# Kernel tuning notes

Measured on AMD Instinct MI355X. Metric: run time of the kernel, lower is better.

Reference implementation:

```python
import jax, jax.numpy as jnp
import numpy as np

BN_EPS = 1e-5
POOL_TARGETS = (1500, 750, 375)


def mesh_conv(x, nb, W, g, b):
    # x: (E, C), nb: (E, 4), W: (5*C, Cout)
    E, C = x.shape
    n = x[jnp.clip(nb, 0, E - 1)]              # (E, 4, C) gather
    p1 = jnp.sort(n[:, :2, :], axis=1)          # symmetrize face-pair 1
    p2 = jnp.sort(n[:, 2:, :], axis=1)          # symmetrize face-pair 2
    feat = jnp.concatenate([x, p1[:, 0], p1[:, 1], p2[:, 0], p2[:, 1]], axis=1)  # (E, 5C)
    h = feat @ W                                # (E, Cout)
    mu = h.mean(axis=0)
    var = h.var(axis=0)                         # biased var (BatchNorm training stats)
    h = (h - mu) * jax.lax.rsqrt(var + BN_EPS) * g + b
    return jax.nn.relu(h)


def mesh_pool(x, nb, target):
    E = x.shape[0]
    scores = jnp.linalg.norm(x, axis=1)
    keep = jnp.sort(jnp.argsort(-scores)[:target])          # (target,) sorted kept edges
    x_pool = x[keep]
    remap = jnp.full((E,), -1, dtype=jnp.int32).at[keep].set(jnp.arange(target, dtype=jnp.int32))
    nbr = remap[jnp.clip(nb[keep], 0, E - 1)]               # (target, 4)
    self_idx = jnp.broadcast_to(jnp.arange(target, dtype=jnp.int32)[:, None], nbr.shape)
    nb_pool = jnp.where(nbr < 0, self_idx, nbr)
    return x_pool, nb_pool, keep


def mesh_unpool(x_coarse, keep, E_fine):
    # keep is sorted ascending; nearest kept edge by integer index distance
    # (ties -> lower index, matching torch argmin-first semantics).
    idx = jnp.arange(E_fine)
    pos = jnp.searchsorted(keep, idx)
    K = keep.shape[0]
    left = jnp.clip(pos - 1, 0, K - 1)
    right = jnp.clip(pos, 0, K - 1)
    dl = jnp.abs(idx - keep[left])
    dr = jnp.abs(idx - keep[right])
    nn_idx = jnp.where(dl <= dr, left, right)
    return x_coarse[nn_idx]                                 # kept edges map to themselves (d=0)


def setup_inputs() -> dict:
    key = jax.random.key(0)
    ks = jax.random.split(key, 20)
    E = 200000
    x = jax.random.normal(ks[0], (E, 5), dtype=jnp.float32)
    nb = jax.random.randint(ks[1], (E, 4), 0, E, dtype=jnp.int64)

    def lin(k, cin, cout):
        return (jax.random.normal(k, (cin, cout), dtype=jnp.float32) * 0.05)

    dims = [(5, 64), (64, 128), (128, 256), (256, 512), (768, 256), (384, 128), (192, 64)]
    names = ['e1', 'e2', 'e3', 'e4', 'd3', 'd2', 'd1']
    inp = {'x': x, 'nb': nb}
    for i, ((cin, cout), nm) in enumerate(zip(dims, names)):
        inp['W_' + nm] = lin(ks[2 + i], cin * 5, cout)
        inp['g_' + nm] = jnp.ones((cout,), dtype=jnp.float32)
        inp['b_' + nm] = jnp.zeros((cout,), dtype=jnp.float32)
    inp['W_head'] = lin(ks[12], 64, 4)
    inp['bias_head'] = jnp.zeros((4,), dtype=jnp.float32)
    return inp


def _forward(x, nb,
             W_e1, g_e1, b_e1, W_e2, g_e2, b_e2, W_e3, g_e3, b_e3, W_e4, g_e4, b_e4,
             W_d3, g_d3, b_d3, W_d2, g_d2, b_d2, W_d1, g_d1, b_d1,
             W_head, bias_head):
    e1 = mesh_conv(x, nb, W_e1, g_e1, b_e1)
    e1p, nb1, keep1 = mesh_pool(e1, nb, POOL_TARGETS[0])
    e2 = mesh_conv(e1p, nb1, W_e2, g_e2, b_e2)
    e2p, nb2, keep2 = mesh_pool(e2, nb1, POOL_TARGETS[1])
    e3 = mesh_conv(e2p, nb2, W_e3, g_e3, b_e3)
    e3p, nb3, keep3 = mesh_pool(e3, nb2, POOL_TARGETS[2])
    e4 = mesh_conv(e3p, nb3, W_e4, g_e4, b_e4)
    d3 = mesh_unpool(e4, keep3, e3.shape[0])
    d3 = mesh_conv(jnp.concatenate([d3, e3], axis=1), nb2, W_d3, g_d3, b_d3)
    d2 = mesh_unpool(d3, keep2, e2.shape[0])
    d2 = mesh_conv(jnp.concatenate([d2, e2], axis=1), nb1, W_d2, g_d2, b_d2)
    d1 = mesh_unpool(d2, keep1, e1.shape[0])
    d1 = mesh_conv(jnp.concatenate([d1, e1], axis=1), nb, W_d1, g_d1, b_d1)
    return d1 @ W_head + bias_head


def reference(x, nb,
              W_e1, g_e1, b_e1, W_e2, g_e2, b_e2, W_e3, g_e3, b_e3, W_e4, g_e4, b_e4,
              W_d3, g_d3, b_d3, W_d2, g_d2, b_d2, W_d1, g_d1, b_d1,
              W_head, bias_head):
    return _forward(x, nb,
                    W_e1, g_e1, b_e1, W_e2, g_e2, b_e2, W_e3, g_e3, b_e3, W_e4, g_e4, b_e4,
                    W_d3, g_d3, b_d3, W_d2, g_d2, b_d2, W_d1, g_d1, b_d1,
                    W_head, bias_head)
```

## Files before the change

### kernel.cpp

```cpp
#include <hip/hip_runtime.h>
#include <stdint.h>

typedef unsigned long long u64;
typedef unsigned int u32;
typedef unsigned short ushort_t;

#define FI __device__ __forceinline__

static constexpr float BN_EPS_F = 1e-5f;
static constexpr int E0 = 200000;
static constexpr int T1 = 1500, T2 = 750, T3 = 375;
static constexpr int CAND_CAP = 4096;
static constexpr int NB_KEEP = (E0 + 1023) / 1024;

typedef __attribute__((ext_vector_type(8))) short short8;
typedef __attribute__((ext_vector_type(4))) float f32x4;

FI int iclampi(int v, int lo, int hi) { return v < lo ? lo : (v > hi ? hi : v); }

FI ushort_t f2b(float f) {
  u32 u = __float_as_uint(f);
  u32 r = (u + 0x7FFFu + ((u >> 16) & 1u)) >> 16;
  return (ushort_t)r;
}

FI void u16minmax(const uint4& va, const uint4& vb, uint4& lo, uint4& hi) {
  const ushort_t* a = (const ushort_t*)&va;
  const ushort_t* b = (const ushort_t*)&vb;
  ushort_t* l = (ushort_t*)&lo;
  ushort_t* h = (ushort_t*)&hi;
  #pragma unroll
  for (int i = 0; i < 8; i++) {
    ushort_t x = a[i], y = b[i];
    l[i] = x < y ? x : y;
    h[i] = x < y ? y : x;
  }
}

FI int nearest_keep(const int* __restrict__ keep, int K, int idx) {
  int lo = 0, hi = K;
  while (lo < hi) { int mid = (lo + hi) >> 1; if (keep[mid] < idx) lo = mid + 1; else hi = mid; }
  int l = lo - 1; l = l < 0 ? 0 : (l > K - 1 ? K - 1 : l);
  int r = lo;     r = r < 0 ? 0 : (r > K - 1 ? K - 1 : r);
  int dl = idx - keep[l]; dl = dl < 0 ? -dl : dl;
  int dr = idx - keep[r]; dr = dr < 0 ? -dr : dr;
  return (dl <= dr) ? l : r;
}

FI int bsearch_eq(const int* __restrict__ keep, int K, int v) {
  int lo = 0, hi = K;
  while (lo < hi) { int mid = (lo + hi) >> 1; if (keep[mid] < v) lo = mid + 1; else hi = mid; }
  if (lo < K && keep[lo] == v) return lo;
  return -1;
}

template<int C, int Cout, int BR, int BC, int KT, int TR, int TC, int KSPLIT,
         bool FUSE_STATS>
__global__ __launch_bounds__((BR / TR) * (BC / TC))
void conv_kernel(const float* __restrict__ X,
                 const int* __restrict__ nb, int E,
                 const float* __restrict__ W,
                 float* __restrict__ H, float* __restrict__ stats)
{
  constexpr int NTH = (BR / TR) * (BC / TC);
  constexpr int VK = 5 * KT;
  constexpr int KC = C / KSPLIT;
  static_assert(KC % KT == 0, "KC % KT");

  const int row0 = blockIdx.x * BR;
  const int col0 = blockIdx.y * BC;
  const int c_begin = (KSPLIT > 1) ? (int)blockIdx.z * KC : 0;

  __shared__ float As[VK][BR];
  __shared__ float Bs[VK][BC];
  __shared__ int rowsS[5][BR];
  __shared__ float red[FUSE_STATS ? 2 * (BR / TR) * BC : 1];

  const int tid = threadIdx.x;

  for (int q = tid; q < BR; q += NTH) {
    int r = row0 + q;
    int rr[5];
    if (r < E) {
      rr[0] = r;
      #pragma unroll
      for (int j = 0; j < 4; j++) {
        int v = nb[(size_t)r * 4 + j];
        rr[1 + j] = iclampi(v, 0, E - 1);
      }
    } else {
      #pragma unroll
      for (int j = 0; j < 5; j++) rr[j] = -1;
    }
    #pragma unroll
    for (int j = 0; j < 5; j++) rowsS[j][q] = rr[j];
  }

  float acc[TR][TC];
  #pragma unroll
  for (int i = 0; i < TR; i++)
    #pragma unroll
    for (int j = 0; j < TC; j++) acc[i][j] = 0.f;

  const int tr = tid / (BC / TC);
  const int tc = tid % (BC / TC);
  const int rA = tr * TR;
  const int cB = tc * TC;

  for (int c0 = c_begin; c0 < c_begin + KC; c0 += KT) {
    __syncthreads();
    for (int q = tid; q < VK * (BC / 4); q += NTH) {
      int kk = q / (BC / 4);
      int c4 = q % (BC / 4);
      int p = kk / KT, t = kk % KT;
      float4 wv = *(const float4*)&W[(size_t)(p * C + c0 + t) * Cout + col0 + c4 * 4];
      *(float4*)&Bs[kk][c4 * 4] = wv;
    }
    for (int q = tid; q < BR * KT; q += NTH) {
      int t = q % KT, rq = q / KT;
      int c = c0 + t;
      float s0 = 0.f, a1 = 0.f, a2 = 0.f, a3 = 0.f, a4 = 0.f;
      if (rowsS[0][rq] >= 0) {
        float v0, v1, v2, v3;
        s0 = X[(size_t)rowsS[0][rq] * C + c];
        v0 = X[(size_t)rowsS[1][rq] * C + c];
        v1 = X[(size_t)rowsS[2][rq] * C + c];
        v2 = X[(size_t)rowsS[3][rq] * C + c];
        v3 = X[(size_t)rowsS[4][rq] * C + c];
        a1 = fminf(v0, v1); a2 = fmaxf(v0, v1);
        a3 = fminf(v2, v3); a4 = fmaxf(v2, v3);
      }
      As[0 * KT + t][rq] = s0;
      As[1 * KT + t][rq] = a1;
      As[2 * KT + t][rq] = a2;
      As[3 * KT + t][rq] = a3;
      As[4 * KT + t][rq] = a4;
    }
    __syncthreads();

    for (int kk = 0; kk < VK; kk++) {
      float a[TR], b[TC];
      #pragma unroll
      for (int i = 0; i < TR; i++) a[i] = As[kk][rA + i];
      #pragma unroll
      for (int j = 0; j < TC; j++) b[j] = Bs[kk][cB + j];
      #pragma unroll
      for (int i = 0; i < TR; i++)
        #pragma unroll
        for (int j = 0; j < TC; j++)
          acc[i][j] = fmaf(a[i], b[j], acc[i][j]);
    }
  }

  #pragma unroll
  for (int i = 0; i < TR; i++) {
    int r = row0 + rA + i;
    if (r < E) {
      if constexpr (KSPLIT > 1) {
        #pragma unroll
        for (int j = 0; j < TC; j++)
          atomicAdd(&H[(size_t)r * Cout + col0 + cB + j], acc[i][j]);
      } else {
        #pragma unroll
        for (int j = 0; j < TC; j += 4) {
          float4 v = make_float4(acc[i][j], acc[i][j + 1], acc[i][j + 2], acc[i][j + 3]);
          *(float4*)&H[(size_t)r * Cout + col0 + cB + j] = v;
        }
      }
    }
  }

  if constexpr (FUSE_STATS) {
    float s[TC], q2[TC];
    #pragma unroll
    for (int j = 0; j < TC; j++) { s[j] = 0.f; q2[j] = 0.f; }
    #pragma unroll
    for (int i = 0; i < TR; i++) {
      int r = row0 + rA + i;
      if (r < E) {
        #pragma unroll
        for (int j = 0; j < TC; j++) { float v = acc[i][j]; s[j] += v; q2[j] += v * v; }
      }
    }
    __syncthreads();
    float* redS = &red[0];
    float* redQ = &red[(BR / TR) * BC];
    #pragma unroll
    for (int j = 0; j < TC; j++) {
      redS[tr * BC + cB + j] = s[j];
      redQ[tr * BC + cB + j] = q2[j];
    }
    __syncthreads();
    for (int col = tid; col < BC; col += NTH) {
      float ts = 0.f, tq = 0.f;
      for (int g = 0; g < BR / TR; g++) { ts += redS[g * BC + col]; tq += redQ[g * BC + col]; }
      atomicAdd(&stats[col0 + col], ts);
      atomicAdd(&stats[Cout + col0 + col], tq);
    }
  }
}

__global__ __launch_bounds__(256)
void e1_conv_kernel(const float* __restrict__ X, const int* __restrict__ nb,
                    const float* __restrict__ W,
                    float* __restrict__ H, float* __restrict__ stats)
{
  __shared__ float As[25][128];
  __shared__ float Bs[25][64];
  __shared__ float red[2 * 32 * 64];

  const int tid = threadIdx.x;
  const int row0 = (int)blockIdx.x * 128;

  if (tid < 128) {
    int r = row0 + tid; if (r > E0 - 1) r = E0 - 1;
    int rs[5];
    rs[0] = r;
    #pragma unroll
    for (int j = 0; j < 4; j++) rs[1 + j] = iclampi((int)nb[(size_t)r * 4 + j], 0, E0 - 1);
    float v[5][5];
    #pragma unroll
    for (int j = 0; j < 5; j++) {
      const float* src = &X[(size_t)rs[j] * 5];
      float4 a = *(const float4*)src;
      v[j][0] = a.x; v[j][1] = a.y; v[j][2] = a.z; v[j][3] = a.w;
      v[j][4] = src[4];
    }
    #pragma unroll
    for (int c = 0; c < 5; c++) {
      As[0 * 5 + c][tid] = v[0][c];
      As[1 * 5 + c][tid] = fminf(v[1][c], v[2][c]);
      As[2 * 5 + c][tid] = fmaxf(v[1][c], v[2][c]);
      As[3 * 5 + c][tid] = fminf(v[3][c], v[4][c]);
      As[4 * 5 + c][tid] = fmaxf(v[3][c], v[4][c]);
    }
  } else {
    for (int q = tid - 128; q < 25 * 16; q += 128) {
      int k = q / 16, c4 = q % 16;
      float4 wv = *(const float4*)&W[(size_t)k * 64 + c4 * 4];
      *(float4*)&Bs[k][c4 * 4] = wv;
    }
  }
  __syncthreads();

  const int tr = tid >> 3;
  const int tc = tid & 7;
  const int rA = tr * 4;
  const int cB = tc * 8;

  float acc[4][8];
  #pragma unroll
  for (int i = 0; i < 4; i++)
    #pragma unroll
    for (int j = 0; j < 8; j++) acc[i][j] = 0.f;

  for (int k = 0; k < 25; k++) {
    float a[4], b[8];
    #pragma unroll
    for (int i = 0; i < 4; i++) a[i] = As[k][rA + i];
    #pragma unroll
    for (int j = 0; j < 8; j++) b[j] = Bs[k][cB + j];
    #pragma unroll
    for (int i = 0; i < 4; i++)
      #pragma unroll
      for (int j = 0; j < 8; j++)
        acc[i][j] = fmaf(a[i], b[j], acc[i][j]);
  }

  float s[8], q2[8];
  #pragma unroll
  for (int j = 0; j < 8; j++) { s[j] = 0.f; q2[j] = 0.f; }
  #pragma unroll
  for (int i = 0; i < 4; i++) {
    int r = row0 + rA + i;
    if (r < E0) {
      #pragma unroll
      for (int j = 0; j < 8; j += 4) {
        float4 v = make_float4(acc[i][j], acc[i][j + 1], acc[i][j + 2], acc[i][j + 3]);
        *(float4*)&H[(size_t)r * 64 + cB + j] = v;
      }
      #pragma unroll
      for (int j = 0; j < 8; j++) { float v = acc[i][j]; s[j] += v; q2[j] += v * v; }
    }
  }
  __syncthreads();
  float* redS = &red[0];
  float* redQ = &red[32 * 64];
  #pragma unroll
  for (int j = 0; j < 8; j++) {
    redS[tr * 64 + cB + j] = s[j];
    redQ[tr * 64 + cB + j] = q2[j];
  }
  __syncthreads();
  for (int col = tid; col < 64; col += 256) {
    float ts = 0.f, tq = 0.f;
    for (int g = 0; g < 32; g++) { ts += redS[g * 64 + col]; tq += redQ[g * 64 + col]; }
    atomicAdd(&stats[col], ts);
    atomicAdd(&stats[64 + col], tq);
  }
}

template<int C, int Cout>
__global__ __launch_bounds__(128)
void mfma_conv_kernel(const ushort_t* __restrict__ src,
                      const int* __restrict__ nb, int E,
                      const ushort_t* __restrict__ Wt,
                      float* __restrict__ H, float* __restrict__ stats)
{
  constexpr int NCC = C / 32;
  __shared__ int rows[5][32];

  const int tid = threadIdx.x;
  const int lane = tid & 63;
  const int wv = tid >> 6;
  const int l15 = lane & 15;
  const int quad = lane >> 4;
  const int row0 = (int)blockIdx.x * 32;
  const int col0 = (int)blockIdx.y * 64;

  if (tid < 32) {
    int r = row0 + tid; if (r > E - 1) r = E - 1;
    rows[0][tid] = r;
    #pragma unroll
    for (int j = 0; j < 4; j++) rows[1 + j][tid] = iclampi(nb[(size_t)r * 4 + j], 0, E - 1);
  }
  __syncthreads();

  const int rr = wv * 16 + l15;
  int r5[5];
  #pragma unroll
  for (int j = 0; j < 5; j++) r5[j] = rows[j][rr];

  f32x4 acc[4];
  #pragma unroll
  for (int ni = 0; ni < 4; ni++) acc[ni] = (f32x4){0.f, 0.f, 0.f, 0.f};

  uint4 raw[2][5];
  auto loadcc = [&](int par, int cc2) {
    int cb = cc2 * 32 + quad * 8;
    #pragma unroll
    for (int j = 0; j < 5; j++)
      raw[par][j] = *(const uint4*)&src[(size_t)r5[j] * C + cb];
  };

  loadcc(0, 0);
  #pragma unroll
  for (int cc = 0; cc < NCC; cc++) {
    const int par = cc & 1;
    if (cc + 1 < NCC) loadcc(par ^ 1, cc + 1);
    short8 a[5];
    a[0] = *(short8*)&raw[par][0];
    {
      uint4 lo, hi;
      u16minmax(raw[par][1], raw[par][2], lo, hi);
      a[1] = *(short8*)&lo; a[2] = *(short8*)&hi;
    }
    {
      uint4 lo, hi;
      u16minmax(raw[par][3], raw[par][4], lo, hi);
      a[3] = *(short8*)&lo; a[4] = *(short8*)&hi;
    }
    #pragma unroll
    for (int p = 0; p < 5; p++) {
      #pragma unroll
      for (int ni = 0; ni < 4; ni++) {
        short8 bf = *(const short8*)&Wt[((size_t)(p * Cout + col0 + ni * 16 + l15)) * C + cc * 32 + quad * 8];
        acc[ni] = __builtin_amdgcn_mfma_f32_16x16x32_bf16(a[p], bf, acc[ni], 0, 0, 0);
      }
    }
  }

  float s[4] = {0.f, 0.f, 0.f, 0.f}, q[4] = {0.f, 0.f, 0.f, 0.f};
  #pragma unroll
  for (int reg = 0; reg < 4; reg++) {
    int r = row0 + wv * 16 + quad * 4 + reg;
    if (r < E) {
      #pragma unroll
      for (int ni = 0; ni < 4; ni++) {
        float v = acc[ni][reg];
        H[(size_t)r * Cout + col0 + ni * 16 + l15] = v;
        s[ni] += v; q[ni] += v * v;
      }
    }
  }
  #pragma unroll
  for (int ni = 0; ni < 4; ni++) {
    float ts = s[ni], tq = q[ni];
    ts += __shfl_xor(ts, 16); tq += __shfl_xor(tq, 16);
    ts += __shfl_xor(ts, 32); tq += __shfl_xor(tq, 32);
    if (quad == 0) {
      int col = col0 + ni * 16 + l15;
      atomicAdd(&stats[col], ts);
      atomicAdd(&stats[Cout + col], tq);
    }
  }
}

__global__ __launch_bounds__(256, 4)
void d1_mfma_kernel(const ushort_t* __restrict__ d2b, const ushort_t* __restrict__ e1b,
                    const int* __restrict__ nn1, const int* __restrict__ nb,
                    const ushort_t* __restrict__ Wt,
                    float* __restrict__ H, float* __restrict__ stats)
{
  __shared__ int rowsD[5][128];
  __shared__ int rowsS[5][128];

  const int tid = threadIdx.x;
  const int lane = tid & 63;
  const int wv = tid >> 6;
  const int l15 = lane & 15;
  const int quad = lane >> 4;
  const int row0 = (int)blockIdx.x * 128;

  if (tid < 128) {
    int r = row0 + tid; if (r > E0 - 1) r = E0 - 1;
    int rs[5];
    rs[0] = r;
    #pragma unroll
    for (int j = 0; j < 4; j++) rs[1 + j] = iclampi((int)nb[(size_t)r * 4 + j], 0, E0 - 1);
    #pragma unroll
    for (int j = 0; j < 5; j++) { rowsS[j][tid] = rs[j]; rowsD[j][tid] = nn1[rs[j]]; }
  }
  __syncthreads();

  f32x4 acc[8];
  #pragma unroll
  for (int mi = 0; mi < 8; mi++) acc[mi] = (f32x4){0.f, 0.f, 0.f, 0.f};

  for (int cc = 0; cc < 6; cc++) {
    const bool fromD = cc < 4;
    const ushort_t* __restrict__ src = fromD ? d2b : e1b;
    const int stride = fromD ? 128 : 64;
    const int cbase = (fromD ? cc * 32 : (cc - 4) * 32) + quad * 8;

    short8 bf[5];
    #pragma unroll
    for (int p = 0; p < 5; p++)
      bf[p] = *(const short8*)&Wt[((size_t)(p * 64 + wv * 16 + l15)) * 192 + cc * 32 + quad * 8];

    #pragma unroll 2
    for (int mi = 0; mi < 8; mi++) {
      int rr = mi * 16 + l15;
      int r0, r1, r2, r3, r4;
      if (fromD) {
        r0 = rowsD[0][rr]; r1 = rowsD[1][rr]; r2 = rowsD[2][rr];
        r3 = rowsD[3][rr]; r4 = rowsD[4][rr];
      } else {
        r0 = rowsS[0][rr]; r1 = rowsS[1][rr]; r2 = rowsS[2][rr];
        r3 = rowsS[3][rr]; r4 = rowsS[4][rr];
      }
      uint4 v0 = *(const uint4*)&src[(size_t)r0 * stride + cbase];
      uint4 v1 = *(const uint4*)&src[(size_t)r1 * stride + cbase];
      uint4 v2 = *(const uint4*)&src[(size_t)r2 * stride + cbase];
      uint4 v3 = *(const uint4*)&src[(size_t)r3 * stride + cbase];
      uint4 v4 = *(const uint4*)&src[(size_t)r4 * stride + cbase];

      uint4 lo12, hi12, lo34, hi34;
      u16minmax(v1, v2, lo12, hi12);
      u16minmax(v3, v4, lo34, hi34);

      acc[mi] = __builtin_amdgcn_mfma_f32_16x16x32_bf16(*(short8*)&v0,   bf[0], acc[mi], 0, 0, 0);
      acc[mi] = __builtin_amdgcn_mfma_f32_16x16x32_bf16(*(short8*)&lo12, bf[1], acc[mi], 0, 0, 0);
      acc[mi] = __builtin_amdgcn_mfma_f32_16x16x32_bf16(*(short8*)&hi12, bf[2], acc[mi], 0, 0, 0);
      acc[mi] = __builtin_amdgcn_mfma_f32_16x16x32_bf16(*(short8*)&lo34, bf[3], acc[mi], 0, 0, 0);
      acc[mi] = __builtin_amdgcn_mfma_f32_16x16x32_bf16(*(short8*)&hi34, bf[4], acc[mi], 0, 0, 0);
    }
  }

  const int col = wv * 16 + l15;
  float s = 0.f, q = 0.f;
  #pragma unroll
  for (int mi = 0; mi < 8; mi++) {
    #pragma unroll
    for (int reg = 0; reg < 4; reg++) {
      int r = row0 + mi * 16 + quad * 4 + reg;
      if (r < E0) {
        float v = acc[mi][reg];
        H[(size_t)r * 64 + col] = v;
        s += v; q += v * v;
      }
    }
  }
  s += __shfl_xor(s, 16); q += __shfl_xor(q, 16);
  s += __shfl_xor(s, 32); q += __shfl_xor(q, 32);
  if (quad == 0) {
    atomicAdd(&stats[col], s);
    atomicAdd(&stats[64 + col], q);
  }
}

template<int C, int Cout>
__global__ void prep_w_kernel(const float* __restrict__ W, ushort_t* __restrict__ Wt)
{
  int idx = (int)blockIdx.x * 256 + threadIdx.x;
  if (idx < 5 * C * Cout) {
    int n = idx % Cout;
    int k = idx / Cout;
    int p = k / C, c = k % C;
    Wt[((size_t)(p * Cout + n)) * C + c] = f2b(W[(size_t)k * Cout + n]);
  }
}

__global__ void stats_kernel(const float* __restrict__ H, int E, int Cout,
                             float* __restrict__ stats)
{
  const int RB = 64;
  int r0 = (int)blockIdx.x * RB;
  int rend = r0 + RB; if (rend > E) rend = E;
  for (int col = threadIdx.x; col < Cout; col += blockDim.x) {
    float s = 0.f, q = 0.f;
    for (int r = r0; r < rend; r++) { float v = H[(size_t)r * Cout + col]; s += v; q += v * v; }
    atomicAdd(&stats[col], s);
    atomicAdd(&stats[Cout + col], q);
  }
}

template<int Cout, bool KEYS, bool B16>
__global__ void bn_kernel(const float* __restrict__ H, const float* __restrict__ stats,
                          const float* __restrict__ g, const float* __restrict__ b,
                          int E, float* __restrict__ Out, ushort_t* __restrict__ Outb,
                          u64* __restrict__ keys)
{
  constexpr int CPL = Cout / 64;
  const int lane = threadIdx.x & 63;
  const int wid = threadIdx.x >> 6;
  const int wpb = blockDim.x >> 6;
  const float invE = 1.0f / (float)E;
  float mu[CPL], inv[CPL], gg[CPL], bb[CPL];
  #pragma unroll
  for (int u = 0; u < CPL; u++) {
    int c = lane + u * 64;
    float m = stats[c] * invE;
    float var = stats[Cout + c] * invE - m * m;
    mu[u] = m;
    inv[u] = rsqrtf(var + BN_EPS_F);
    gg[u] = g[c]; bb[u] = b[c];
  }
  for (int r = (int)blockIdx.x * wpb + wid; r < E; r += (int)gridDim.x * wpb) {
    float ss = 0.f;
    #pragma unroll
    for (int u = 0; u < CPL; u++) {
      int c = lane + u * 64;
      float v = H[(size_t)r * Cout + c];
      float o = (v - mu[u]) * inv[u] * gg[u] + bb[u];
      o = fmaxf(o, 0.f);
      Out[(size_t)r * Cout + c] = o;
      if constexpr (B16) Outb[(size_t)r * Cout + c] = f2b(o);
      ss += o * o;
    }
    if constexpr (KEYS) {
      #pragma unroll
      for (int s = 32; s > 0; s >>= 1) ss += __shfl_xor(ss, s, 64);
      if (lane == 0) {
        float sc = sqrtf(ss);
        u32 sb = __float_as_uint(sc);
        keys[r] = ((u64)sb << 32) | (u64)(0xFFFFFFFFu - (u32)r);
      }
    }
  }
}

__global__ void head_kernel(const float* __restrict__ H, const float* __restrict__ stats,
                            const float* __restrict__ g, const float* __restrict__ b,
                            const float* __restrict__ Wh, const float* __restrict__ bh,
                            int E, float* __restrict__ out)
{
  const int lane = threadIdx.x & 63;
  const int wid = threadIdx.x >> 6;
  const int wpb = blockDim.x >> 6;
  const float invE = 1.0f / (float)E;
  float m = stats[lane] * invE;
  float var = stats[64 + lane] * invE - m * m;
  float inv = rsqrtf(var + BN_EPS_F);
  float gg = g[lane], bb = b[lane];
  float4 w = *(const float4*)&Wh[lane * 4];
  float b0 = bh[0], b1 = bh[1], b2 = bh[2], b3 = bh[3];
  for (int r = (int)blockIdx.x * wpb + wid; r < E; r += (int)gridDim.x * wpb) {
    float v = H[(size_t)r * 64 + lane];
    float o = fmaxf((v - m) * inv * gg + bb, 0.f);
    float a0 = o * w.x, a1 = o * w.y, a2 = o * w.z, a3 = o * w.w;
    #pragma unroll
    for (int s = 32; s > 0; s >>= 1) {
      a0 += __shfl_xor(a0, s, 64);
      a1 += __shfl_xor(a1, s, 64);
      a2 += __shfl_xor(a2, s, 64);
      a3 += __shfl_xor(a3, s, 64);
    }
    if (lane == 0) {
      float4 ov = make_float4(a0 + b0, a1 + b1, a2 + b2, a3 + b3);
      *(float4*)&out[(size_t)r * 4] = ov;
    }
  }
}

__global__ void hist_kernel(const u64* __restrict__ keys, int E, u32* __restrict__ hist)
{
  for (int i = (int)blockIdx.x * blockDim.x + threadIdx.x; i < E;
       i += (int)gridDim.x * blockDim.x) {
    u32 bin = (u32)(keys[i] >> 44);
    atomicAdd(&hist[bin], 1u);
  }
}

__global__ void scan_kernel(const u32* __restrict__ hist, int K, u32* __restrict__ sel)
{
  __shared__ u32 csum[1024];
  __shared__ u32 sb2[1024];
  __shared__ int selChunk;
  __shared__ u32 aboveChunk;
  const int tid = threadIdx.x;
  {
    const uint4* hp = (const uint4*)(hist + (size_t)tid * 1024);
    u32 s = 0;
    for (int i = 0; i < 256; i++) {
      uint4 v = hp[i];
      s += v.x + v.y + v.z + v.w;
    }
    csum[tid] = s;
  }
  __syncthreads();
  if (tid == 0) {
    u32 above = 0; int sc = 0; u32 ab = 0;
    for (int t = 1023; t >= 0; t--) {
      if (above + csum[t] >= (u32)K) { sc = t; ab = above; break; }
      above += csum[t];
    }
    selChunk = sc; aboveChunk = ab;
  }
  __syncthreads();
  sb2[tid] = hist[(size_t)selChunk * 1024 + tid];
  __syncthreads();
  if (tid == 0) {
    u32 above = aboveChunk; int sb = 0;
    for (int t = 1023; t >= 0; t--) {
      u32 c = sb2[t];
      if (above + c >= (u32)K) { sb = t; break; }
      above += c;
    }
    sel[0] = (u32)(selChunk * 1024 + sb);
    sel[1] = above;
    sel[2] = (u32)K - above;
  }
}

__global__ void collect_kernel(const u64* __restrict__ keys, int E, const u32* __restrict__ sel,
                               u64* __restrict__ cand, u32* __restrict__ count)
{
  u32 bin = sel[0];
  for (int i = (int)blockIdx.x * blockDim.x + threadIdx.x; i < E;
       i += (int)gridDim.x * blockDim.x) {
    if ((u32)(keys[i] >> 44) == bin) {
      u32 p = atomicAdd(count, 1u);
      if (p < (u32)CAND_CAP) cand[p] = keys[i];
    }
  }
}

__global__ void thresh_kernel(const u64* __restrict__ cand, const u32* __restrict__ count,
                              const u32* __restrict__ sel, u64* __restrict__ thr)
{
  __shared__ u64 sk[CAND_CAP];
  const int tid = threadIdx.x;
  const int nth = blockDim.x;
  int n = (int)(*count > (u32)CAND_CAP ? (u32)CAND_CAP : *count);
  int n2 = 2; while (n2 < n) n2 <<= 1;
  for (int i = tid; i < n2; i += nth) sk[i] = (i < n) ? cand[i] : 0ull;
  __syncthreads();
  for (int k = 2; k <= n2; k <<= 1)
    for (int j = k >> 1; j > 0; j >>= 1) {
      for (int i = tid; i < n2; i += nth) {
        int p = i ^ j;
        if (p > i) {
          u64 a = sk[i], bb = sk[p];
          bool up = ((i & k) == 0);
          bool sw = up ? (a < bb) : (a > bb);
          if (sw) { sk[i] = bb; sk[p] = a; }
        }
      }
      __syncthreads();
    }
  if (tid == 0) {
    int kr = (int)sel[2];
    thr[0] = sk[kr - 1];
  }
}

__global__ void keep_count_kernel(const u64* __restrict__ keys, int E,
                                  const u64* __restrict__ thrp, u32* __restrict__ bcnt)
{
  const u64 thr = thrp[0];
  const int tid = threadIdx.x;
  int base = (int)blockIdx.x * 1024 + tid * 4;
  u32 c = 0;
  #pragma unroll
  for (int u = 0; u < 4; u++) {
    int i = base + u;
    if (i < E && keys[i] >= thr) c++;
  }
  __shared__ u32 sm[256];
  sm[tid] = c;
  __syncthreads();
  for (int s = 128; s > 0; s >>= 1) {
    if (tid < s) sm[tid] += sm[tid + s];
    __syncthreads();
  }
  if (tid == 0) bcnt[blockIdx.x] = sm[0];
}

__global__ void keep_scan_kernel(const u32* __restrict__ bcnt, int NB, u32* __restrict__ boffs)
{
  __shared__ u32 sm[256];
  const int tid = threadIdx.x;
  u32 v = (tid < NB) ? bcnt[tid] : 0;
  sm[tid] = v;
  __syncthreads();
  for (int off = 1; off < 256; off <<= 1) {
    u32 t = 0;
    if (tid >= off) t = sm[tid - off];
    __syncthreads();
    sm[tid] += t;
    __syncthreads();
  }
  if (tid < NB) boffs[tid] = sm[tid] - v;
}

__global__ void keep_scatter_kernel(const u64* __restrict__ keys, int E,
                                    const u64* __restrict__ thrp, const u32* __restrict__ boffs,
                                    int* __restrict__ keep, int K)
{
  const u64 thr = thrp[0];
  const int tid = threadIdx.x;
  int base = (int)blockIdx.x * 1024 + tid * 4;
  u32 f[4]; u32 c = 0;
  #pragma unroll
  for (int u = 0; u < 4; u++) {
    int i = base + u;
    f[u] = (i < E && keys[i] >= thr) ? 1u : 0u;
    c += f[u];
  }
  __shared__ u32 sm[256];
  sm[tid] = c;
  __syncthreads();
  for (int off = 1; off < 256; off <<= 1) {
    u32 t = 0;
    if (tid >= off) t = sm[tid - off];
    __syncthreads();
    sm[tid] += t;
    __syncthreads();
  }
  u32 pos = boffs[blockIdx.x] + sm[tid] - c;
  #pragma unroll
  for (int u = 0; u < 4; u++) {
    if (f[u]) {
      if (pos < (u32)K) keep[pos] = base + u;
      pos++;
    }
  }
}

template<int NPOW>
__global__ void pool_select_kernel(const u64* __restrict__ keys, int E, int K,
                                   int* __restrict__ keep)
{
  __shared__ u64 sk[NPOW];
  __shared__ int si[NPOW];
  const int tid = threadIdx.x, nth = blockDim.x;
  for (int i = tid; i < NPOW; i += nth) sk[i] = (i < E) ? keys[i] : 0ull;
  __syncthreads();
  for (int k = 2; k <= NPOW; k <<= 1)
    for (int j = k >> 1; j > 0; j >>= 1) {
      for (int i = tid; i < NPOW; i += nth) {
        int p = i ^ j;
        if (p > i) {
          u64 a = sk[i], bb = sk[p];
          bool up = ((i & k) == 0);
          bool sw = up ? (a < bb) : (a > bb);
          if (sw) { sk[i] = bb; sk[p] = a; }
        }
      }
      __syncthreads();
    }
  for (int i = tid; i < NPOW; i += nth)
    si[i] = (i < K) ? (int)(0xFFFFFFFFu - (u32)(sk[i] & 0xFFFFFFFFull)) : 0x7FFFFFFF;
  __syncthreads();
  for (int k = 2; k <= NPOW; k <<= 1)
    for (int j = k >> 1; j > 0; j >>= 1) {
      for (int i = tid; i < NPOW; i += nth) {
        int p = i ^ j;
        if (p > i) {
          int a = si[i], bb = si[p];
          bool up = ((i & k) == 0);
          bool sw = up ? (a > bb) : (a < bb);
          if (sw) { si[i] = bb; si[p] = a; }
        }
      }
      __syncthreads();
    }
  for (int i = tid; i < K; i += nth) keep[i] = si[i];
}

template<int C, bool B16>
__global__ void pool_finish_kernel(const float* __restrict__ Xsrc, const int* __restrict__ nb_src,
                                   const int* __restrict__ keep, int K, int Esrc,
                                   float* __restrict__ Xp, ushort_t* __restrict__ Xpb,
                                   int* __restrict__ nbp)
{
  int total = K * C;
  for (int idx = (int)blockIdx.x * blockDim.x + threadIdx.x; idx < total;
       idx += (int)gridDim.x * blockDim.x) {
    int i = idx / C, c = idx % C;
    float v = Xsrc[(size_t)keep[i] * C + c];
    if constexpr (B16) Xpb[idx] = f2b(v);
    else Xp[idx] = v;
  }
  for (int idx = (int)blockIdx.x * blockDim.x + threadIdx.x; idx < K * 4;
       idx += (int)gridDim.x * blockDim.x) {
    int i = idx >> 2, j = idx & 3;
    int v = nb_src[(size_t)keep[i] * 4 + j];
    v = iclampi(v, 0, Esrc - 1);
    int p = bsearch_eq(keep, K, v);
    nbp[idx] = (p < 0) ? i : p;
  }
}

__global__ void unpool_cat_b16_kernel(const float* __restrict__ Xc, const float* __restrict__ Xs,
                                      const int* __restrict__ keep, int K, int E,
                                      int Cc, int Cs, ushort_t* __restrict__ out)
{
  int Ct = Cc + Cs;
  int total = E * Ct;
  for (int idx = (int)blockIdx.x * blockDim.x + threadIdx.x; idx < total;
       idx += (int)gridDim.x * blockDim.x) {
    int r = idx / Ct, c = idx % Ct;
    float v;
    if (c < Cc) { int nn = nearest_keep(keep, K, r); v = Xc[(size_t)nn * Cc + c]; }
    else v = Xs[(size_t)r * Cs + (c - Cc)];
    out[idx] = f2b(v);
  }
}

__global__ void nn_map_kernel(const int* __restrict__ keep, int K, int E, int* __restrict__ nn)
{
  for (int i = (int)blockIdx.x * blockDim.x + threadIdx.x; i < E;
       i += (int)gridDim.x * blockDim.x)
    nn[i] = nearest_keep(keep, K, i);
}

extern "C" void kernel_launch(void* const* d_in, const int* in_sizes, int n_in,
                              void* d_out, int out_size, void* d_ws, size_t ws_size,
                              hipStream_t stream)
{
  (void)in_sizes; (void)n_in; (void)out_size; (void)ws_size;
  const float* x     = (const float*)d_in[0];
  const int*   nb    = (const int*)d_in[1];
  const float* W_e1  = (const float*)d_in[2];
  const float* g_e1  = (const float*)d_in[3];
  const float* b_e1  = (const float*)d_in[4];
  const float* W_e2  = (const float*)d_in[5];
  const float* g_e2  = (const float*)d_in[6];
  const float* b_e2  = (const float*)d_in[7];
  const float* W_e3  = (const float*)d_in[8];
  const float* g_e3  = (const float*)d_in[9];
  const float* b_e3  = (const float*)d_in[10];
  const float* W_e4  = (const float*)d_in[11];
  const float* g_e4  = (const float*)d_in[12];
  const float* b_e4  = (const float*)d_in[13];
  const float* W_d3  = (const float*)d_in[14];
  const float* g_d3  = (const float*)d_in[15];
  const float* b_d3  = (const float*)d_in[16];
  const float* W_d2  = (const float*)d_in[17];
  const float* g_d2  = (const float*)d_in[18];
  const float* b_d2  = (const float*)d_in[19];
  const float* W_d1  = (const float*)d_in[20];
  const float* g_d1  = (const float*)d_in[21];
  const float* b_d1  = (const float*)d_in[22];
  const float* W_head = (const float*)d_in[23];
  const float* bias_head = (const float*)d_in[24];
  float* out = (float*)d_out;

  char* p = (char*)d_ws;
  auto alloc = [&](size_t bytes) -> char* {
    char* q = p; p += (bytes + 255) & ~(size_t)255; return q;
  };

  char* zz = p;
  u32*   hist  = (u32*)alloc(sizeof(u32) * (1u << 20));
  float* stats = (float*)alloc(sizeof(float) * 2 * (64 + 128 + 256 + 512 + 256 + 128 + 64));
  u32*   ctrl  = (u32*)alloc(sizeof(u32) * 16);
  u64*   thr   = (u64*)alloc(sizeof(u64) * 2);
  u32*   sel   = (u32*)alloc(sizeof(u32) * 8);
  float* H2    = (float*)alloc(sizeof(float) * T1 * 128);
  float* H3    = (float*)alloc(sizeof(float) * T2 * 256);
  size_t zz_bytes = (size_t)(p - zz);
  float* H4    = (float*)alloc(sizeof(float) * T3 * 512);
  float* Hd3   = (float*)alloc(sizeof(float) * T2 * 256);
  float* Hd2   = (float*)alloc(sizeof(float) * T1 * 128);
  u32*   bcnt  = (u32*)alloc(sizeof(u32) * 256);
  u32*   boffs = (u32*)alloc(sizeof(u32) * 256);
  float* e1    = (float*)alloc(sizeof(float) * (size_t)E0 * 64);
  u64*   keys1 = (u64*)alloc(sizeof(u64) * E0);
  u64*   cand  = (u64*)alloc(sizeof(u64) * CAND_CAP);
  int*   keep1 = (int*)alloc(sizeof(int) * T1);
  float* e1p   = (float*)alloc(sizeof(float) * T1 * 64);
  int*   nb1   = (int*)alloc(sizeof(int) * T1 * 4);
  float* e2    = (float*)alloc(sizeof(float) * T1 * 128);
  u64*   keys2 = (u64*)alloc(sizeof(u64) * T1);
  int*   keep2 = (int*)alloc(sizeof(int) * T2);
  float* e2p   = (float*)alloc(sizeof(float) * T2 * 128);
  int*   nb2   = (int*)alloc(sizeof(int) * T2 * 4);
  float* e3    = (float*)alloc(sizeof(float) * T2 * 256);
  u64*   keys3 = (u64*)alloc(sizeof(u64) * T2);
  int*   keep3 = (int*)alloc(sizeof(int) * T3);
  ushort_t* e3pb = (ushort_t*)alloc(sizeof(ushort_t) * T3 * 256);
  int*   nb3   = (int*)alloc(sizeof(int) * T3 * 4);
  float* e4    = (float*)alloc(sizeof(float) * T3 * 512);
  ushort_t* d3catb = (ushort_t*)alloc(sizeof(ushort_t) * T2 * 768);
  float* d3    = (float*)alloc(sizeof(float) * T2 * 256);
  ushort_t* d2catb = (ushort_t*)alloc(sizeof(ushort_t) * T1 * 384);
  float* d2    = (float*)alloc(sizeof(float) * T1 * 128);
  int*   nn1   = (int*)alloc(sizeof(int) * E0);
  float* Hd1   = (float*)alloc(sizeof(float) * (size_t)E0 * 64);
  ushort_t* e1b = (ushort_t*)alloc(sizeof(ushort_t) * (size_t)E0 * 64);
  ushort_t* d2b = (ushort_t*)alloc(sizeof(ushort_t) * T1 * 128);
  ushort_t* Wt1 = (ushort_t*)alloc(sizeof(ushort_t) * 5 * 64 * 192);
  ushort_t* Wt4 = (ushort_t*)alloc(sizeof(ushort_t) * 5 * 512 * 256);
  ushort_t* Wtd3 = (ushort_t*)alloc(sizeof(ushort_t) * 5 * 256 * 768);
  ushort_t* Wtd2 = (ushort_t*)alloc(sizeof(ushort_t) * 5 * 128 * 384);

  float* s1  = stats;
  float* s2  = s1 + 2 * 64;
  float* s3  = s2 + 2 * 128;
  float* s4  = s3 + 2 * 256;
  float* sd3 = s4 + 2 * 512;
  float* sd2 = sd3 + 2 * 256;
  float* sd1 = sd2 + 2 * 128;

  hipMemsetAsync(zz, 0, zz_bytes, stream);
  prep_w_kernel<192, 64><<<dim3((5 * 192 * 64 + 255) / 256), 256, 0, stream>>>(W_d1, Wt1);
  prep_w_kernel<256, 512><<<dim3((5 * 256 * 512 + 255) / 256), 256, 0, stream>>>(W_e4, Wt4);
  prep_w_kernel<768, 256><<<dim3((5 * 768 * 256 + 255) / 256), 256, 0, stream>>>(W_d3, Wtd3);
  prep_w_kernel<384, 128><<<dim3((5 * 384 * 128 + 255) / 256), 256, 0, stream>>>(W_d2, Wtd2);

  e1_conv_kernel<<<dim3((E0 + 127) / 128), 256, 0, stream>>>(x, nb, W_e1, e1, s1);
  bn_kernel<64, true, true><<<dim3(8192), 256, 0, stream>>>(e1, s1, g_e1, b_e1, E0, e1, e1b, keys1);

  hist_kernel<<<dim3(782), 256, 0, stream>>>(keys1, E0, hist);
  scan_kernel<<<dim3(1), 1024, 0, stream>>>(hist, T1, sel);
  collect_kernel<<<dim3(782), 256, 0, stream>>>(keys1, E0, sel, cand, ctrl);
  thresh_kernel<<<dim3(1), 1024, 0, stream>>>(cand, ctrl, sel, thr);
  keep_count_kernel<<<dim3(NB_KEEP), 256, 0, stream>>>(keys1, E0, thr, bcnt);
  keep_scan_kernel<<<dim3(1), 256, 0, stream>>>(bcnt, NB_KEEP, boffs);
  keep_scatter_kernel<<<dim3(NB_KEEP), 256, 0, stream>>>(keys1, E0, thr, boffs, keep1, T1);
  pool_finish_kernel<64, false><<<dim3(380), 256, 0, stream>>>(e1, nb, keep1, T1, E0, e1p, nullptr, nb1);

  conv_kernel<64, 128, 32, 64, 8, 2, 4, 2, false>
      <<<dim3((T1 + 31) / 32, 128 / 64, 2), 256, 0, stream>>>(e1p, nb1, T1, W_e2, H2, nullptr);
  stats_kernel<<<dim3((T1 + 63) / 64), 256, 0, stream>>>(H2, T1, 128, s2);
  bn_kernel<128, true, false><<<dim3(512), 256, 0, stream>>>(H2, s2, g_e2, b_e2, T1, e2, nullptr, keys2);
  pool_select_kernel<2048><<<dim3(1), 256, 0, stream>>>(keys2, T1, T2, keep2);
  pool_finish_kernel<128, false><<<dim3(380), 256, 0, stream>>>(e2, nb1, keep2, T2, T1, e2p, nullptr, nb2);

  conv_kernel<128, 256, 32, 64, 8, 2, 4, 4, false>
      <<<dim3((T2 + 31) / 32, 256 / 64, 4), 256, 0, stream>>>(e2p, nb2, T2, W_e3, H3, nullptr);
  stats_kernel<<<dim3((T2 + 63) / 64), 256, 0, stream>>>(H3, T2, 256, s3);
  bn_kernel<256, true, false><<<dim3(256), 256, 0, stream>>>(H3, s3, g_e3, b_e3, T2, e3, nullptr, keys3);
  pool_select_kernel<1024><<<dim3(1), 256, 0, stream>>>(keys3, T2, T3, keep3);
  pool_finish_kernel<256, true><<<dim3(380), 256, 0, stream>>>(e3, nb2, keep3, T3, T2, nullptr, e3pb, nb3);

  mfma_conv_kernel<256, 512><<<dim3((T3 + 31) / 32, 512 / 64), 128, 0, stream>>>(
      e3pb, nb3, T3, Wt4, H4, s4);
  bn_kernel<512, false, false><<<dim3(128), 256, 0, stream>>>(
      H4, s4, g_e4, b_e4, T3, e4, nullptr, nullptr);

  unpool_cat_b16_kernel<<<dim3((T2 * 768 + 255) / 256), 256, 0, stream>>>(
      e4, e3, keep3, T3, T2, 512, 256, d3catb);
  mfma_conv_kernel<768, 256><<<dim3((T2 + 31) / 32, 256 / 64), 128, 0, stream>>>(
      d3catb, nb2, T2, Wtd3, Hd3, sd3);
  bn_kernel<256, false, false><<<dim3(256), 256, 0, stream>>>(
      Hd3, sd3, g_d3, b_d3, T2, d3, nullptr, nullptr);

  unpool_cat_b16_kernel<<<dim3((T1 * 384 + 255) / 256), 256, 0, stream>>>(
      d3, e2, keep2, T2, T1, 256, 128, d2catb);
  mfma_conv_kernel<384, 128><<<dim3((T1 + 31) / 32, 128 / 64), 128, 0, stream>>>(
      d2catb, nb1, T1, Wtd2, Hd2, sd2);
  bn_kernel<128, false, true><<<dim3(512), 256, 0, stream>>>(
      Hd2, sd2, g_d2, b_d2, T1, d2, d2b, nullptr);

  nn_map_kernel<<<dim3(782), 256, 0, stream>>>(keep1, T1, E0, nn1);
  d1_mfma_kernel<<<dim3((E0 + 127) / 128), 256, 0, stream>>>(d2b, e1b, nn1, nb, Wt1, Hd1, sd1);

  head_kernel<<<dim3(8192), 256, 0, stream>>>(Hd1, sd1, g_d1, b_d1, W_head, bias_head, E0, out);
}
```

Baseline: 1.111 ms.

## Split-K the small MFMA convs, merge weight prep, vectorize unpool-concat

The small-row MFMA conv kernels now split their K dimension across blockIdx.z and accumulate into a zeroed H buffer with atomics. Batch-norm statistics move out of those kernels into separate stats_kernel launches. The four weight-prep launches become one combined kernel, unpool_cat writes eight bf16 values per thread with vector loads, and pool_select runs with 1024 threads. The intent is more parallelism on the tiny decoder and bottleneck layers and fewer launches, at the cost of extra atomics, extra stats launches, and a larger memset range.

```diff
diff --git a/kernel.cpp b/kernel.cpp
--- a/kernel.cpp
+++ b/kernel.cpp
@@ -300,14 +300,16 @@
   }
 }
 
-template<int C, int Cout>
+template<int C, int Cout, int KSPLIT>
 __global__ __launch_bounds__(128)
 void mfma_conv_kernel(const ushort_t* __restrict__ src,
                       const int* __restrict__ nb, int E,
                       const ushort_t* __restrict__ Wt,
-                      float* __restrict__ H, float* __restrict__ stats)
-{
-  constexpr int NCC = C / 32;
+                      float* __restrict__ H)
+{
+  constexpr int NCC_T = C / 32;
+  constexpr int NCC = NCC_T / KSPLIT;
+  static_assert(NCC_T % KSPLIT == 0, "NCC_T % KSPLIT");
   __shared__ int rows[5][32];
 
   const int tid = threadIdx.x;
@@ -317,6 +319,7 @@
   const int quad = lane >> 4;
   const int row0 = (int)blockIdx.x * 32;
   const int col0 = (int)blockIdx.y * 64;
+  const int cc0 = (KSPLIT > 1) ? (int)blockIdx.z * NCC : 0;
 
   if (tid < 32) {
     int r = row0 + tid; if (r > E - 1) r = E - 1;
@@ -337,7 +340,7 @@
 
   uint4 raw[2][5];
   auto loadcc = [&](int par, int cc2) {
-    int cb = cc2 * 32 + quad * 8;
+    int cb = (cc0 + cc2) * 32 + quad * 8;
     #pragma unroll
     for (int j = 0; j < 5; j++)
       raw[par][j] = *(const uint4*)&src[(size_t)r5[j] * C + cb];
@@ -364,34 +367,23 @@
     for (int p = 0; p < 5; p++) {
       #pragma unroll
       for (int ni = 0; ni < 4; ni++) {
-        short8 bf = *(const short8*)&Wt[((size_t)(p * Cout + col0 + ni * 16 + l15)) * C + cc * 32 + quad * 8];
+        short8 bf = *(const short8*)&Wt[((size_t)(p * Cout + col0 + ni * 16 + l15)) * C + (cc0 + cc) * 32 + quad * 8];
         acc[ni] = __builtin_amdgcn_mfma_f32_16x16x32_bf16(a[p], bf, acc[ni], 0, 0, 0);
       }
     }
   }
 
-  float s[4] = {0.f, 0.f, 0.f, 0.f}, q[4] = {0.f, 0.f, 0.f, 0.f};
   #pragma unroll
   for (int reg = 0; reg < 4; reg++) {
     int r = row0 + wv * 16 + quad * 4 + reg;
     if (r < E) {
       #pragma unroll
       for (int ni = 0; ni < 4; ni++) {
-        float v = acc[ni][reg];
-        H[(size_t)r * Cout + col0 + ni * 16 + l15] = v;
-        s[ni] += v; q[ni] += v * v;
-      }
-    }
-  }
-  #pragma unroll
-  for (int ni = 0; ni < 4; ni++) {
-    float ts = s[ni], tq = q[ni];
-    ts += __shfl_xor(ts, 16); tq += __shfl_xor(tq, 16);
-    ts += __shfl_xor(ts, 32); tq += __shfl_xor(tq, 32);
-    if (quad == 0) {
-      int col = col0 + ni * 16 + l15;
-      atomicAdd(&stats[col], ts);
-      atomicAdd(&stats[Cout + col], tq);
+        if constexpr (KSPLIT > 1)
+          atomicAdd(&H[(size_t)r * Cout + col0 + ni * 16 + l15], acc[ni][reg]);
+        else
+          H[(size_t)r * Cout + col0 + ni * 16 + l15] = acc[ni][reg];
+      }
     }
   }
 }
@@ -489,16 +481,29 @@
   }
 }
 
-template<int C, int Cout>
-__global__ void prep_w_kernel(const float* __restrict__ W, ushort_t* __restrict__ Wt)
+FI void prep_one(const float* __restrict__ W, ushort_t* __restrict__ Wt,
+                 int C, int Cout, int i)
+{
+  int n = i % Cout;
+  int k = i / Cout;
+  int p = k / C, c = k % C;
+  Wt[((size_t)(p * Cout + n)) * C + c] = f2b(W[(size_t)k * Cout + n]);
+}
+
+__global__ void prep_all_kernel(const float* __restrict__ W1, const float* __restrict__ W4,
+                                const float* __restrict__ Wd3, const float* __restrict__ Wd2,
+                                ushort_t* __restrict__ Wt1, ushort_t* __restrict__ Wt4,
+                                ushort_t* __restrict__ Wtd3, ushort_t* __restrict__ Wtd2)
 {
   int idx = (int)blockIdx.x * 256 + threadIdx.x;
-  if (idx < 5 * C * Cout) {
-    int n = idx % Cout;
-    int k = idx / Cout;
-    int p = k / C, c = k % C;
-    Wt[((size_t)(p * Cout + n)) * C + c] = f2b(W[(size_t)k * Cout + n]);
-  }
+  const int S1 = 5 * 192 * 64, S4 = 5 * 256 * 512, Sd3 = 5 * 768 * 256, Sd2 = 5 * 384 * 128;
+  if (idx < S1) { prep_one(W1, Wt1, 192, 64, idx); return; }
+  idx -= S1;
+  if (idx < S4) { prep_one(W4, Wt4, 256, 512, idx); return; }
+  idx -= S4;
+  if (idx < Sd3) { prep_one(Wd3, Wtd3, 768, 256, idx); return; }
+  idx -= Sd3;
+  if (idx < Sd2) { prep_one(Wd2, Wtd2, 384, 128, idx); return; }
 }
 
 __global__ void stats_kernel(const float* __restrict__ H, int E, int Cout,
@@ -828,14 +833,20 @@
                                       int Cc, int Cs, ushort_t* __restrict__ out)
 {
   int Ct = Cc + Cs;
-  int total = E * Ct;
+  int Ct8 = Ct >> 3;
+  int total = E * Ct8;
   for (int idx = (int)blockIdx.x * blockDim.x + threadIdx.x; idx < total;
        idx += (int)gridDim.x * blockDim.x) {
-    int r = idx / Ct, c = idx % Ct;
-    float v;
-    if (c < Cc) { int nn = nearest_keep(keep, K, r); v = Xc[(size_t)nn * Cc + c]; }
-    else v = Xs[(size_t)r * Cs + (c - Cc)];
-    out[idx] = f2b(v);
+    int r = idx / Ct8, c = (idx % Ct8) << 3;
+    const float* srcp;
+    if (c < Cc) { int nn = nearest_keep(keep, K, r); srcp = &Xc[(size_t)nn * Cc + c]; }
+    else srcp = &Xs[(size_t)r * Cs + (c - Cc)];
+    float4 a = *(const float4*)srcp;
+    float4 b = *(const float4*)(srcp + 4);
+    ushort_t o[8];
+    o[0] = f2b(a.x); o[1] = f2b(a.y); o[2] = f2b(a.z); o[3] = f2b(a.w);
+    o[4] = f2b(b.x); o[5] = f2b(b.y); o[6] = f2b(b.z); o[7] = f2b(b.w);
+    *(uint4*)&out[(size_t)r * Ct + c] = *(uint4*)o;
   }
 }
 
@@ -891,10 +902,10 @@
   u32*   sel   = (u32*)alloc(sizeof(u32) * 8);
   float* H2    = (float*)alloc(sizeof(float) * T1 * 128);
   float* H3    = (float*)alloc(sizeof(float) * T2 * 256);
-  size_t zz_bytes = (size_t)(p - zz);
   float* H4    = (float*)alloc(sizeof(float) * T3 * 512);
   float* Hd3   = (float*)alloc(sizeof(float) * T2 * 256);
   float* Hd2   = (float*)alloc(sizeof(float) * T1 * 128);
+  size_t zz_bytes = (size_t)(p - zz);
   u32*   bcnt  = (u32*)alloc(sizeof(u32) * 256);
   u32*   boffs = (u32*)alloc(sizeof(u32) * 256);
   float* e1    = (float*)alloc(sizeof(float) * (size_t)E0 * 64);
@@ -936,10 +947,9 @@
   float* sd1 = sd2 + 2 * 128;
 
   hipMemsetAsync(zz, 0, zz_bytes, stream);
-  prep_w_kernel<192, 64><<<dim3((5 * 192 * 64 + 255) / 256), 256, 0, stream>>>(W_d1, Wt1);
-  prep_w_kernel<256, 512><<<dim3((5 * 256 * 512 + 255) / 256), 256, 0, stream>>>(W_e4, Wt4);
-  prep_w_kernel<768, 256><<<dim3((5 * 768 * 256 + 255) / 256), 256, 0, stream>>>(W_d3, Wtd3);
-  prep_w_kernel<384, 128><<<dim3((5 * 384 * 128 + 255) / 256), 256, 0, stream>>>(W_d2, Wtd2);
+  const int PREP_TOTAL = 5 * (192 * 64 + 256 * 512 + 768 * 256 + 384 * 128);
+  prep_all_kernel<<<dim3((PREP_TOTAL + 255) / 256), 256, 0, stream>>>(
+      W_d1, W_e4, W_d3, W_d2, Wt1, Wt4, Wtd3, Wtd2);
 
   e1_conv_kernel<<<dim3((E0 + 127) / 128), 256, 0, stream>>>(x, nb, W_e1, e1, s1);
   bn_kernel<64, true, true><<<dim3(8192), 256, 0, stream>>>(e1, s1, g_e1, b_e1, E0, e1, e1b, keys1);
@@ -957,32 +967,35 @@
       <<<dim3((T1 + 31) / 32, 128 / 64, 2), 256, 0, stream>>>(e1p, nb1, T1, W_e2, H2, nullptr);
   stats_kernel<<<dim3((T1 + 63) / 64), 256, 0, stream>>>(H2, T1, 128, s2);
   bn_kernel<128, true, false><<<dim3(512), 256, 0, stream>>>(H2, s2, g_e2, b_e2, T1, e2, nullptr, keys2);
-  pool_select_kernel<2048><<<dim3(1), 256, 0, stream>>>(keys2, T1, T2, keep2);
+  pool_select_kernel<2048><<<dim3(1), 1024, 0, stream>>>(keys2, T1, T2, keep2);
   pool_finish_kernel<128, false><<<dim3(380), 256, 0, stream>>>(e2, nb1, keep2, T2, T1, e2p, nullptr, nb2);
 
   conv_kernel<128, 256, 32, 64, 8, 2, 4, 4, false>
       <<<dim3((T2 + 31) / 32, 256 / 64, 4), 256, 0, stream>>>(e2p, nb2, T2, W_e3, H3, nullptr);
   stats_kernel<<<dim3((T2 + 63) / 64), 256, 0, stream>>>(H3, T2, 256, s3);
   bn_kernel<256, true, false><<<dim3(256), 256, 0, stream>>>(H3, s3, g_e3, b_e3, T2, e3, nullptr, keys3);
-  pool_select_kernel<1024><<<dim3(1), 256, 0, stream>>>(keys3, T2, T3, keep3);
+  pool_select_kernel<1024><<<dim3(1), 1024, 0, stream>>>(keys3, T2, T3, keep3);
   pool_finish_kernel<256, true><<<dim3(380), 256, 0, stream>>>(e3, nb2, keep3, T3, T2, nullptr, e3pb, nb3);
 
-  mfma_conv_kernel<256, 512><<<dim3((T3 + 31) / 32, 512 / 64), 128, 0, stream>>>(
-      e3pb, nb3, T3, Wt4, H4, s4);
+  mfma_conv_kernel<256, 512, 4><<<dim3((T3 + 31) / 32, 512 / 64, 4), 128, 0, stream>>>(
+      e3pb, nb3, T3, Wt4, H4);
+  stats_kernel<<<dim3((T3 + 63) / 64), 256, 0, stream>>>(H4, T3, 512, s4);
   bn_kernel<512, false, false><<<dim3(128), 256, 0, stream>>>(
       H4, s4, g_e4, b_e4, T3, e4, nullptr, nullptr);
 
-  unpool_cat_b16_kernel<<<dim3((T2 * 768 + 255) / 256), 256, 0, stream>>>(
+  unpool_cat_b16_kernel<<<dim3((T2 * 768 / 8 + 255) / 256), 256, 0, stream>>>(
       e4, e3, keep3, T3, T2, 512, 256, d3catb);
-  mfma_conv_kernel<768, 256><<<dim3((T2 + 31) / 32, 256 / 64), 128, 0, stream>>>(
-      d3catb, nb2, T2, Wtd3, Hd3, sd3);
+  mfma_conv_kernel<768, 256, 6><<<dim3((T2 + 31) / 32, 256 / 64, 6), 128, 0, stream>>>(
+      d3catb, nb2, T2, Wtd3, Hd3);
+  stats_kernel<<<dim3((T2 + 63) / 64), 256, 0, stream>>>(Hd3, T2, 256, sd3);
   bn_kernel<256, false, false><<<dim3(256), 256, 0, stream>>>(
       Hd3, sd3, g_d3, b_d3, T2, d3, nullptr, nullptr);
 
-  unpool_cat_b16_kernel<<<dim3((T1 * 384 + 255) / 256), 256, 0, stream>>>(
+  unpool_cat_b16_kernel<<<dim3((T1 * 384 / 8 + 255) / 256), 256, 0, stream>>>(
       d3, e2, keep2, T2, T1, 256, 128, d2catb);
-  mfma_conv_kernel<384, 128><<<dim3((T1 + 31) / 32, 128 / 64), 128, 0, stream>>>(
-      d2catb, nb1, T1, Wtd2, Hd2, sd2);
+  mfma_conv_kernel<384, 128, 3><<<dim3((T1 + 31) / 32, 128 / 64, 3), 128, 0, stream>>>(
+      d2catb, nb1, T1, Wtd2, Hd2);
+  stats_kernel<<<dim3((T1 + 63) / 64), 256, 0, stream>>>(Hd2, T1, 128, sd2);
   bn_kernel<128, false, true><<<dim3(512), 256, 0, stream>>>(
       Hd2, sd2, g_d2, b_d2, T1, d2, d2b, nullptr);
 
```

After: 987.7 us. 1.13x faster.
